# Optimization experiments

Measured on AMD Instinct MI355X. Metric: run time of the kernel, lower is better.

The kernel has to match this reference:

```python
import jax, jax.numpy as jnp
import numpy as np

SIGNAL = (32, 32)
KERNEL = (8, 8)
N_FEATURES = [64, 128, 128]
BATCH = 64
ALPHA = 0.5          # source references an undefined global `alpha`; fixed here
LEAKY_SLOPE = 0.01   # torch F.leaky_relu default


def _join_tensor(S, K, loc):
    i = np.arange(S)[:, None, None]
    j = np.arange(S)[None, :, None]
    k = np.arange(K)[None, None, :]
    M = (j >= i) & (i == np.maximum(j, k + loc))
    return jnp.asarray(M.astype(np.float32))


def _meet_tensor(S, K, loc):
    i = np.arange(S)[:, None, None]
    j = np.arange(S)[None, :, None]
    k = np.arange(K)[None, None, :]
    M = (j >= i) & (i == np.minimum(j, k + loc))
    return jnp.asarray(M.astype(np.float32))


def setup_inputs() -> dict:
    key = jax.random.key(0)
    sx, sy = SIGNAL
    kx, ky = KERNEL
    # meet layers use kernel_loc = signal - kernel; join layers use (0, 0)
    cmx = _meet_tensor(sx, kx, sx - kx)
    cmy = _meet_tensor(sy, ky, sy - ky)
    cjx = _join_tensor(sx, kx, 0)
    cjy = _join_tensor(sy, ky, 0)

    keys = jax.random.split(key, 16)
    x = jax.random.normal(keys[0], (BATCH, N_FEATURES[0], sx, sy), dtype=jnp.float32)

    def kaiming(k, shape):
        fan_in = shape[0] * shape[1] * shape[2]  # kx*ky*in_features
        return jax.random.normal(k, shape, dtype=jnp.float32) * np.float32(np.sqrt(2.0 / fan_in))

    inp = {"x": x, "cmx": cmx, "cmy": cmy, "cjx": cjx, "cjy": cjy}
    for li in range(len(N_FEATURES) - 1):
        fi, fo = N_FEATURES[li], N_FEATURES[li + 1]
        inp[f"mw{li}"] = kaiming(keys[1 + 2 * li], (kx, ky, fi, fo))
        inp[f"mb{li}"] = jnp.zeros((fo, 1, 1), dtype=jnp.float32)
        inp[f"jw{li}"] = kaiming(keys[2 + 2 * li], (kx, ky, fi, fo))
        inp[f"jb{li}"] = jnp.zeros((fo, 1, 1), dtype=jnp.float32)
    return inp


def _lattice_conv(cx, cy, X, W, b):
    # Y[m,g,x,y] = sum_{i,j,a,b} cx[i,x,a] cy[j,y,b] X[m,f,i,j] W[a,b,f,g] + bias
    return jnp.einsum('ixa,jyb,mfij,abfg->mgxy', cx, cy, X, W, optimize='optimal') + b


def reference(x, cmx, cmy, cjx, cjy, mw0, mb0, jw0, jb0, mw1, mb1, jw1, jb1):
    params = [(mw0, mb0, jw0, jb0), (mw1, mb1, jw1, jb1)]
    for mw, mb, jw, jb in params:
        m = _lattice_conv(cmx, cmy, x, mw, mb)
        j = _lattice_conv(cjx, cjy, x, jw, jb)
        x = jax.nn.leaky_relu((1.0 - ALPHA) * m + ALPHA * j, negative_slope=LEAKY_SLOPE)
    return x
```

## Files before the change

### kernel.cpp

```cpp
#include <hip/hip_runtime.h>
#include <stdint.h>


typedef __attribute__((ext_vector_type(8))) short short8;
typedef __attribute__((ext_vector_type(4))) float floatx4;

__device__ __forceinline__ float bf2f(unsigned short u) {
  union { uint32_t u; float f; } c; c.u = ((uint32_t)u) << 16; return c.f;
}
__device__ __forceinline__ unsigned short f2bf(float f) {
  union { float f; uint32_t u; } c; c.f = f;
  uint32_t u = c.u;
  uint32_t r = (u + 0x7FFFu + ((u >> 16) & 1u)) >> 16;
  return (unsigned short)r;
}

__device__ __forceinline__ int detect_fp32_block(
    const unsigned short* __restrict__ xa, int* scnt) {
  if (threadIdx.x == 0) *scnt = 0;
  __syncthreads();
  unsigned short v = xa[threadIdx.x & 255];
  int e = (v >> 7) & 0xFF;
  int ok = (v == 0) || (e >= 110 && e <= 140);
  atomicAdd(scnt, ok);
  __syncthreads();
  return (*scnt >= 240) ? 0 : 1;
}

#define SLOT_W1 0
#define SLOT_SB 225
#define SLOT_AS 289
#define SLOT_M  353
#define N_SLOTS 417
#define N_SLOTS_PAD 448

__global__ __launch_bounds__(256) void mega_setup(
    const unsigned short* __restrict__ xa,
    const void* __restrict__ mw0, const void* __restrict__ jw0,
    const void* __restrict__ mw1, const void* __restrict__ jw1,
    const void* __restrict__ mb0, const void* __restrict__ jb0,
    const void* __restrict__ mb1, const void* __restrict__ jb1,
    unsigned short* __restrict__ L, float* __restrict__ bias0,
    float* __restrict__ bias1, unsigned short* __restrict__ PBg0,
    unsigned short* __restrict__ PBg1, unsigned short* __restrict__ Xt0) {
  __shared__ unsigned short shbuf[128 * 33];
  __shared__ int scnt;
  int blk = blockIdx.x;

  if (blk < 224) {
    int tid = blk * 256 + threadIdx.x;
    int slot = tid >> 7, k = tid & 127;
    int isj = k >= 64, ab = k & 63, a = ab >> 3, b = ab & 7;
    float v = 0.f;
    if (slot < 225) {
      int cx = slot / 15, cy = slot % 15;
      int pmx = cx < 7 ? cx : 7, pxx = cx > 7 ? cx - 7 : 0;
      int pmy = cy < 7 ? cy : 7, pyy = cy > 7 ? cy - 7 : 0;
      if (!isj) v = (a >= pxx && b >= pyy) ? 0.5f : 0.f;
      else      v = (a <= pmx && b <= pmy) ? 0.5f : 0.f;
    } else if (slot < 289) {
      int s = slot - SLOT_SB, px = s >> 3, b0 = s & 7;
      if (!isj) v = (a >= px && b == b0) ? 0.5f : 0.f;
    } else if (slot < 353) {
      int s = slot - SLOT_AS, a0 = s >> 3, py = s & 7;
      if (!isj) v = (a == a0 && b >= py) ? 0.5f : 0.f;
    } else if (slot < 417) {
      int s = slot - SLOT_M, a0 = s >> 3, b0 = s & 7;
      if (!isj) v = (a == a0 && b == b0) ? 0.5f : 0.f;
    }
    L[tid] = f2bf(v);
    return;
  }

  if (blk == 224) {
    int fp32 = detect_fp32_block(xa, &scnt);
    int g = threadIdx.x & 127;
    const void* mb = (threadIdx.x < 128) ? mb0 : mb1;
    const void* jb = (threadIdx.x < 128) ? jb0 : jb1;
    float* bo = (threadIdx.x < 128) ? bias0 : bias1;
    float m = fp32 ? ((const float*)mb)[g] : bf2f(((const unsigned short*)mb)[g]);
    float j = fp32 ? ((const float*)jb)[g] : bf2f(((const unsigned short*)jb)[g]);
    bo[g] = 0.5f * (m + j);
    return;
  }

  int tx = threadIdx.x & 31, ty = threadIdx.x >> 5;

  if (blk < 1249) {
    int fp32 = detect_fp32_block(xa, &scnt);
    int pblk = blk - 225;
    int layer = pblk >> 9;
    int rem = pblk & 511;
    int f = rem >> 2, gt = rem & 3;
    int F = layer ? 128 : 64;
    if (f >= F) return;
    int g0 = gt * 32;
    const int G = 128, FG = F * G;
    const void* mw = layer ? mw1 : mw0;
    const void* jw = layer ? jw1 : jw0;
    unsigned short* PB = layer ? PBg1 : PBg0;
    for (int k = ty; k < 128; k += 8) {
      const void* src = (k < 64) ? mw : jw;
      int ab = k & 63;
      size_t idx = (size_t)ab * FG + (size_t)f * G + g0 + tx;
      shbuf[k * 33 + tx] = fp32 ? f2bf(((const float*)src)[idx])
                                : ((const unsigned short*)src)[idx];
    }
    __syncthreads();
    int kk = threadIdx.x & 127, gs = threadIdx.x >> 7;
    for (int gg = gs; gg < 32; gg += 2)
      PB[((size_t)(g0 + gg) * F + f) * 128 + kk] = shbuf[kk * 33 + gg];
    return;
  }

  {
    int fp32 = detect_fp32_block(xa, &scnt);
    int tblk = blk - 1249;
    int c0 = (tblk & 31) * 32, r0 = (tblk >> 5) * 32;
    const int R = 4096, C = 1024;
    if (fp32) {
#pragma unroll
      for (int i = 0; i < 32; i += 8)
        shbuf[(ty + i) * 33 + tx] =
            f2bf(((const float*)xa)[(size_t)(r0 + ty + i) * C + (c0 + tx)]);
    } else {
#pragma unroll
      for (int i = 0; i < 32; i += 8)
        shbuf[(ty + i) * 33 + tx] = xa[(size_t)(r0 + ty + i) * C + (c0 + tx)];
    }
    __syncthreads();
#pragma unroll
    for (int i = 0; i < 32; i += 8)
      Xt0[(size_t)(c0 + ty + i) * R + (r0 + tx)] = shbuf[tx * 33 + ty + i];
  }
}

template <int F, int NT>
__device__ __forceinline__ void mfma_tile(
    const unsigned short* __restrict__ A, const unsigned short* __restrict__ W,
    floatx4 acc[NT], int wave, int n, int q) {
  const unsigned short* a_ptr = A + ((size_t)(wave * 16 + n)) * F + q * 8;
  const unsigned short* w_ptr = W + (size_t)n * F + q * 8;
#pragma unroll
  for (int kk = 0; kk < F; kk += 32) {
    short8 av = *(const short8*)(a_ptr + kk);
#pragma unroll
    for (int t = 0; t < NT; ++t) {
      short8 bv = *(const short8*)(w_ptr + (size_t)t * 16 * F + kk);
      acc[t] = __builtin_amdgcn_mfma_f32_16x16x32_bf16(av, bv, acc[t], 0, 0, 0);
    }
  }
}

__global__ __launch_bounds__(256) void prep_gemm2(
    const unsigned short* __restrict__ L,
    const unsigned short* __restrict__ PBg0,
    const unsigned short* __restrict__ PBg1,
    unsigned short* __restrict__ Wall0, unsigned short* __restrict__ Wall1) {
  int layer = blockIdx.z;
  int GF = layer ? 16384 : 8192;
  int n0 = blockIdx.x * 128;
  if (n0 >= GF) return;
  int m0 = blockIdx.y * 64;
  const unsigned short* PB = layer ? PBg1 : PBg0;
  unsigned short* Wall = layer ? Wall1 : Wall0;
  int wave = threadIdx.x >> 6, lane = threadIdx.x & 63;
  int n = lane & 15, q = lane >> 4;
  floatx4 acc[8];
#pragma unroll
  for (int t = 0; t < 8; ++t) acc[t] = (floatx4){0.f, 0.f, 0.f, 0.f};
  mfma_tile<128, 8>(L + (size_t)m0 * 128, PB + (size_t)n0 * 128, acc, wave, n, q);
#pragma unroll
  for (int t = 0; t < 8; ++t) {
    int gcol = n0 + t * 16 + n;
#pragma unroll
    for (int r = 0; r < 4; ++r) {
      int m = m0 + wave * 16 + q * 4 + r;
      Wall[(size_t)m * GF + gcol] = f2bf(acc[t][r]);
    }
  }
}

template <int F>
__global__ __launch_bounds__(256) void corr_gemm(
    const unsigned short* __restrict__ Xt, const unsigned short* __restrict__ Wall,
    unsigned short* __restrict__ V, unsigned short* __restrict__ U,
    unsigned short* __restrict__ T) {
  int bid = blockIdx.x, gs = blockIdx.y;
  int wave = threadIdx.x >> 6, lane = threadIdx.x & 63;
  int n = lane & 15, q = lane >> 4;
  int ipos, slot;
  unsigned short* out;
  if (bid < 256) {
    int a = bid >> 5, y = bid & 31;
    int py = y > 24 ? y - 24 : 0;
    ipos = (24 + a) * 32 + y;
    slot = SLOT_AS + a * 8 + py;
    out = V + (size_t)(a * 32 + y) * 8192;
  } else if (bid < 512) {
    int i = bid - 256;
    int b = i >> 5, x = i & 31;
    int px = x > 24 ? x - 24 : 0;
    ipos = x * 32 + 24 + b;
    slot = SLOT_SB + px * 8 + b;
    out = U + (size_t)(b * 32 + x) * 8192;
  } else {
    int i = bid - 512;
    int a = i >> 3, b = i & 7;
    ipos = (24 + a) * 32 + 24 + b;
    slot = SLOT_M + a * 8 + b;
    out = T + (size_t)(a * 8 + b) * 8192;
  }
  floatx4 acc[4];
#pragma unroll
  for (int t = 0; t < 4; ++t) acc[t] = (floatx4){0.f, 0.f, 0.f, 0.f};
  mfma_tile<F, 4>(Xt + (size_t)ipos * 64 * F,
                  Wall + ((size_t)slot * 128 + gs * 64) * F, acc, wave, n, q);
#pragma unroll
  for (int t = 0; t < 4; ++t) {
    int gcol = gs * 64 + t * 16 + n;
#pragma unroll
    for (int r = 0; r < 4; ++r) {
      int m = wave * 16 + q * 4 + r;
      out[(size_t)m * 128 + gcol] = f2bf(acc[t][r]);
    }
  }
}

__global__ __launch_bounds__(256) void scan_corr(unsigned short* __restrict__ V,
                                                 unsigned short* __restrict__ U,
                                                 unsigned short* __restrict__ T) {
  int b = blockIdx.x;
  if (b < 2048) {
    unsigned short* base = (b < 1024) ? V : U;
    int tid = ((b & 1023) * 256 + threadIdx.x);
    unsigned short* p = base + (size_t)tid;
    float s = 0.f;
#pragma unroll
    for (int a = 0; a < 8; ++a) {
      s += bf2f(p[(size_t)a * 262144]);
      p[(size_t)a * 262144] = f2bf(s);
    }
  } else {
    int mg = (b - 2048) * 256 + threadIdx.x;
    float col[8];
#pragma unroll
    for (int i = 0; i < 8; ++i) col[i] = 0.f;
#pragma unroll
    for (int a = 0; a < 8; ++a) {
      float rs = 0.f;
#pragma unroll
      for (int bb = 0; bb < 8; ++bb) {
        size_t idx = (size_t)(a * 8 + bb) * 8192 + mg;
        col[bb] += bf2f(T[idx]);
        rs += col[bb];
        T[idx] = f2bf(rs);
      }
    }
  }
}

template <int F>
__global__ __launch_bounds__(256) void final_gemm(
    const unsigned short* __restrict__ Xt, const unsigned short* __restrict__ Wall,
    const unsigned short* __restrict__ V, const unsigned short* __restrict__ U,
    const unsigned short* __restrict__ T, const float* __restrict__ bias,
    unsigned short* __restrict__ Out) {
  int pos = blockIdx.x, gs = blockIdx.y;
  int x = pos >> 5, y = pos & 31;
  int wave = threadIdx.x >> 6, lane = threadIdx.x & 63;
  int n = lane & 15, q = lane >> 4;
  int clsx = x < 7 ? x : (x <= 24 ? 7 : x - 17);
  int clsy = y < 7 ? y : (y <= 24 ? 7 : y - 17);
  int px = x > 24 ? x - 24 : 0;
  int py = y > 24 ? y - 24 : 0;
  const unsigned short* c3 = px ? V + ((size_t)(px - 1) * 32 + y) * 8192 : nullptr;
  const unsigned short* c2 = py ? U + ((size_t)(py - 1) * 32 + x) * 8192 : nullptr;
  const unsigned short* c4 =
      (px && py) ? T + (size_t)((px - 1) * 8 + (py - 1)) * 8192 : nullptr;

  float csum[4][4];
#pragma unroll
  for (int t = 0; t < 4; ++t) {
    int gcol = gs * 64 + t * 16 + n;
    float bv = bias[gcol];
#pragma unroll
    for (int r = 0; r < 4; ++r) {
      int m = wave * 16 + q * 4 + r;
      size_t idx = (size_t)m * 128 + gcol;
      float v = bv;
      if (c3) v += bf2f(c3[idx]);
      if (c2) v += bf2f(c2[idx]);
      if (c4) v += bf2f(c4[idx]);
      csum[t][r] = v;
    }
  }

  floatx4 acc[4];
#pragma unroll
  for (int t = 0; t < 4; ++t) acc[t] = (floatx4){0.f, 0.f, 0.f, 0.f};
  mfma_tile<F, 4>(Xt + (size_t)pos * 64 * F,
                  Wall + ((size_t)(SLOT_W1 + clsx * 15 + clsy) * 128 + gs * 64) * F,
                  acc, wave, n, q);

  unsigned short* o = Out + (size_t)pos * 64 * 128;
#pragma unroll
  for (int t = 0; t < 4; ++t) {
    int gcol = gs * 64 + t * 16 + n;
#pragma unroll
    for (int r = 0; r < 4; ++r) {
      int m = wave * 16 + q * 4 + r;
      float v = acc[t][r] + csum[t][r];
      v = v > 0.f ? v : 0.01f * v;
      o[(size_t)m * 128 + gcol] = f2bf(v);
    }
  }
}

__global__ __launch_bounds__(256) void transpose_out(
    const unsigned short* __restrict__ xa, const unsigned short* __restrict__ src,
    unsigned short* __restrict__ d16, float* __restrict__ d32) {
  __shared__ unsigned short tile[32][33];
  __shared__ int scnt;
  int fp32 = detect_fp32_block(xa, &scnt);
  const int R = 1024, C = 8192;
  int tx = threadIdx.x & 31, ty = threadIdx.x >> 5;
  int c0 = blockIdx.x * 32, r0 = blockIdx.y * 32;
#pragma unroll
  for (int i = 0; i < 32; i += 8)
    tile[ty + i][tx] = src[(size_t)(r0 + ty + i) * C + (c0 + tx)];
  __syncthreads();
  if (fp32) {
#pragma unroll
    for (int i = 0; i < 32; i += 8)
      d32[(size_t)(c0 + ty + i) * R + (r0 + tx)] = bf2f(tile[tx][ty + i]);
  } else {
#pragma unroll
    for (int i = 0; i < 32; i += 8)
      d16[(size_t)(c0 + ty + i) * R + (r0 + tx)] = tile[tx][ty + i];
  }
}

extern "C" void kernel_launch(void* const* d_in, const int* in_sizes, int n_in,
                              void* d_out, int out_size, void* d_ws,
                              size_t ws_size, hipStream_t stream) {
  const void* x   = d_in[0];
  const void* mw0 = d_in[5];
  const void* mb0 = d_in[6];
  const void* jw0 = d_in[7];
  const void* jb0 = d_in[8];
  const void* mw1 = d_in[9];
  const void* mb1 = d_in[10];
  const void* jw1 = d_in[11];
  const void* jb1 = d_in[12];

  char* ws = (char*)d_ws;
  const size_t MB = 1u << 20;
  unsigned short* Xt0   = (unsigned short*)(ws + 0);
  unsigned short* A1    = (unsigned short*)(ws + 9 * MB);
  unsigned short* Wall0 = (unsigned short*)(ws + 26 * MB);
  unsigned short* Wall1 = (unsigned short*)(ws + 34 * MB);
  unsigned short* Out2  = (unsigned short*)(ws + 49 * MB);
  unsigned short* PBg0  = (unsigned short*)(ws + 66 * MB);
  unsigned short* PBg1  = (unsigned short*)(ws + 69 * MB);
  unsigned short* L     = (unsigned short*)(ws + 74 * MB);
  float* bias0 = (float*)(ws + 75 * MB);
  float* bias1 = bias0 + 128;
  unsigned short* V = (unsigned short*)(ws + 76 * MB);
  unsigned short* U = (unsigned short*)(ws + 81 * MB);
  unsigned short* T = (unsigned short*)(ws + 86 * MB);

  mega_setup<<<5345, 256, 0, stream>>>(
      (const unsigned short*)x, mw0, jw0, mw1, jw1, mb0, jb0, mb1, jb1, L,
      bias0, bias1, PBg0, PBg1, Xt0);
  prep_gemm2<<<dim3(128, 7, 2), 256, 0, stream>>>(L, PBg0, PBg1, Wall0, Wall1);

  corr_gemm<64><<<dim3(576, 2), 256, 0, stream>>>(Xt0, Wall0, V, U, T);
  scan_corr<<<2080, 256, 0, stream>>>(V, U, T);
  final_gemm<64><<<dim3(1024, 2), 256, 0, stream>>>(Xt0, Wall0, V, U, T,
                                                    bias0, A1);
  corr_gemm<128><<<dim3(576, 2), 256, 0, stream>>>(A1, Wall1, V, U, T);
  scan_corr<<<2080, 256, 0, stream>>>(V, U, T);
  final_gemm<128><<<dim3(1024, 2), 256, 0, stream>>>(A1, Wall1, V, U, T,
                                                     bias1, Out2);

  transpose_out<<<dim3(256, 32), 256, 0, stream>>>(
      (const unsigned short*)x, Out2, (unsigned short*)d_out, (float*)d_out);
}
```

Measured before the change: 257.8 us.

## Fuse correction GEMM with prefix scan, accumulating across positions in registers

Merges the corr_gemm and scan_corr kernels: each block iterates over 8 positions along one axis and keeps the MFMA accumulator running, so the stored outputs are already prefix sums. The 2-D scan of the corner tensor T is reduced to a 1-D scan, and final_gemm now sums the needed T slices in a loop. This removes a kernel launch and a read-modify-write pass over V/U/T, but shrinks the grid to 144 blocks with serial work per block and adds extra T reads in final_gemm.

```diff
diff --git a/kernel.cpp b/kernel.cpp
--- a/kernel.cpp
+++ b/kernel.cpp
@@ -182,79 +182,45 @@
 }
 
 template <int F>
-__global__ __launch_bounds__(256) void corr_gemm(
+__global__ __launch_bounds__(256) void corr_scan(
     const unsigned short* __restrict__ Xt, const unsigned short* __restrict__ Wall,
     unsigned short* __restrict__ V, unsigned short* __restrict__ U,
     unsigned short* __restrict__ T) {
   int bid = blockIdx.x, gs = blockIdx.y;
   int wave = threadIdx.x >> 6, lane = threadIdx.x & 63;
   int n = lane & 15, q = lane >> 4;
-  int ipos, slot;
-  unsigned short* out;
-  if (bid < 256) {
-    int a = bid >> 5, y = bid & 31;
-    int py = y > 24 ? y - 24 : 0;
-    ipos = (24 + a) * 32 + y;
-    slot = SLOT_AS + a * 8 + py;
-    out = V + (size_t)(a * 32 + y) * 8192;
-  } else if (bid < 512) {
-    int i = bid - 256;
-    int b = i >> 5, x = i & 31;
-    int px = x > 24 ? x - 24 : 0;
-    ipos = x * 32 + 24 + b;
-    slot = SLOT_SB + px * 8 + b;
-    out = U + (size_t)(b * 32 + x) * 8192;
-  } else {
-    int i = bid - 512;
-    int a = i >> 3, b = i & 7;
-    ipos = (24 + a) * 32 + 24 + b;
-    slot = SLOT_M + a * 8 + b;
-    out = T + (size_t)(a * 8 + b) * 8192;
-  }
   floatx4 acc[4];
 #pragma unroll
   for (int t = 0; t < 4; ++t) acc[t] = (floatx4){0.f, 0.f, 0.f, 0.f};
-  mfma_tile<F, 4>(Xt + (size_t)ipos * 64 * F,
-                  Wall + ((size_t)slot * 128 + gs * 64) * F, acc, wave, n, q);
-#pragma unroll
-  for (int t = 0; t < 4; ++t) {
-    int gcol = gs * 64 + t * 16 + n;
-#pragma unroll
-    for (int r = 0; r < 4; ++r) {
-      int m = wave * 16 + q * 4 + r;
-      out[(size_t)m * 128 + gcol] = f2bf(acc[t][r]);
-    }
-  }
-}
-
-__global__ __launch_bounds__(256) void scan_corr(unsigned short* __restrict__ V,
-                                                 unsigned short* __restrict__ U,
-                                                 unsigned short* __restrict__ T) {
-  int b = blockIdx.x;
-  if (b < 2048) {
-    unsigned short* base = (b < 1024) ? V : U;
-    int tid = ((b & 1023) * 256 + threadIdx.x);
-    unsigned short* p = base + (size_t)tid;
-    float s = 0.f;
-#pragma unroll
-    for (int a = 0; a < 8; ++a) {
-      s += bf2f(p[(size_t)a * 262144]);
-      p[(size_t)a * 262144] = f2bf(s);
-    }
-  } else {
-    int mg = (b - 2048) * 256 + threadIdx.x;
-    float col[8];
-#pragma unroll
-    for (int i = 0; i < 8; ++i) col[i] = 0.f;
-#pragma unroll
-    for (int a = 0; a < 8; ++a) {
-      float rs = 0.f;
-#pragma unroll
-      for (int bb = 0; bb < 8; ++bb) {
-        size_t idx = (size_t)(a * 8 + bb) * 8192 + mg;
-        col[bb] += bf2f(T[idx]);
-        rs += col[bb];
-        T[idx] = f2bf(rs);
+
+  for (int i = 0; i < 8; ++i) {
+    int ipos, slot;
+    unsigned short* out;
+    if (bid < 32) {
+      int y = bid, py = y > 24 ? y - 24 : 0;
+      ipos = (24 + i) * 32 + y;
+      slot = SLOT_AS + i * 8 + py;
+      out = V + (size_t)(i * 32 + y) * 8192;
+    } else if (bid < 64) {
+      int x = bid - 32, px = x > 24 ? x - 24 : 0;
+      ipos = x * 32 + 24 + i;
+      slot = SLOT_SB + px * 8 + i;
+      out = U + (size_t)(i * 32 + x) * 8192;
+    } else {
+      int b = bid - 64;
+      ipos = (24 + i) * 32 + 24 + b;
+      slot = SLOT_M + i * 8 + b;
+      out = T + (size_t)(i * 8 + b) * 8192;
+    }
+    mfma_tile<F, 4>(Xt + (size_t)ipos * 64 * F,
+                    Wall + ((size_t)slot * 128 + gs * 64) * F, acc, wave, n, q);
+#pragma unroll
+    for (int t = 0; t < 4; ++t) {
+      int gcol = gs * 64 + t * 16 + n;
+#pragma unroll
+      for (int r = 0; r < 4; ++r) {
+        int m = wave * 16 + q * 4 + r;
+        out[(size_t)m * 128 + gcol] = f2bf(acc[t][r]);
       }
     }
   }
@@ -276,8 +242,6 @@
   int py = y > 24 ? y - 24 : 0;
   const unsigned short* c3 = px ? V + ((size_t)(px - 1) * 32 + y) * 8192 : nullptr;
   const unsigned short* c2 = py ? U + ((size_t)(py - 1) * 32 + x) * 8192 : nullptr;
-  const unsigned short* c4 =
-      (px && py) ? T + (size_t)((px - 1) * 8 + (py - 1)) * 8192 : nullptr;
 
   float csum[4][4];
 #pragma unroll
@@ -291,8 +255,21 @@
       float v = bv;
       if (c3) v += bf2f(c3[idx]);
       if (c2) v += bf2f(c2[idx]);
-      if (c4) v += bf2f(c4[idx]);
       csum[t][r] = v;
+    }
+  }
+  if (px) {
+    for (int b = 0; b < py; ++b) {
+      const unsigned short* c4 = T + (size_t)((px - 1) * 8 + b) * 8192;
+#pragma unroll
+      for (int t = 0; t < 4; ++t) {
+        int gcol = gs * 64 + t * 16 + n;
+#pragma unroll
+        for (int r = 0; r < 4; ++r) {
+          int m = wave * 16 + q * 4 + r;
+          csum[t][r] += bf2f(c4[(size_t)m * 128 + gcol]);
+        }
+      }
     }
   }
 
@@ -375,12 +352,10 @@
       bias0, bias1, PBg0, PBg1, Xt0);
   prep_gemm2<<<dim3(128, 7, 2), 256, 0, stream>>>(L, PBg0, PBg1, Wall0, Wall1);
 
-  corr_gemm<64><<<dim3(576, 2), 256, 0, stream>>>(Xt0, Wall0, V, U, T);
-  scan_corr<<<2080, 256, 0, stream>>>(V, U, T);
+  corr_scan<64><<<dim3(72, 2), 256, 0, stream>>>(Xt0, Wall0, V, U, T);
   final_gemm<64><<<dim3(1024, 2), 256, 0, stream>>>(Xt0, Wall0, V, U, T,
                                                     bias0, A1);
-  corr_gemm<128><<<dim3(576, 2), 256, 0, stream>>>(A1, Wall1, V, U, T);
-  scan_corr<<<2080, 256, 0, stream>>>(V, U, T);
+  corr_scan<128><<<dim3(72, 2), 256, 0, stream>>>(A1, Wall1, V, U, T);
   final_gemm<128><<<dim3(1024, 2), 256, 0, stream>>>(A1, Wall1, V, U, T,
                                                      bias1, Out2);
 
```

After: 256.9 us. About the same (-0.3%).
